# Kernel tuning notes

Hardware: AMD Instinct MI355X
Metric: run time of the kernel (lower is better)

Reference implementation:

```python
import jax, jax.numpy as jnp
import numpy as np

N = 50000
E = 800000
IN_C = 128
HID_C = 128
OUT_C = 128
N_CLS = 40


def setup_inputs() -> dict:
    key = jax.random.key(0)
    ks = jax.random.split(key, 12)
    x = jax.random.normal(ks[0], (N, IN_C), dtype=jnp.float32)
    edge_index = jax.random.randint(ks[1], (2, E), 0, N, dtype=jnp.int64)
    s = 1.0 / np.sqrt(IN_C)
    W_l1 = jax.random.uniform(ks[2], (IN_C, HID_C), jnp.float32, -s, s)
    W_r1 = jax.random.uniform(ks[3], (IN_C, HID_C), jnp.float32, -s, s)
    b1 = jax.random.uniform(ks[4], (HID_C,), jnp.float32, -s, s)
    s2 = 1.0 / np.sqrt(HID_C)
    W_l2 = jax.random.uniform(ks[5], (HID_C, OUT_C), jnp.float32, -s2, s2)
    W_r2 = jax.random.uniform(ks[6], (HID_C, OUT_C), jnp.float32, -s2, s2)
    b2 = jax.random.uniform(ks[7], (OUT_C,), jnp.float32, -s2, s2)
    s3 = 1.0 / np.sqrt(OUT_C)
    W_c = jax.random.uniform(ks[8], (OUT_C, N_CLS), jnp.float32, -s3, s3)
    b_c = jax.random.uniform(ks[9], (N_CLS,), jnp.float32, -s3, s3)
    return {"x": x, "edge_index": edge_index, "W_l1": W_l1, "W_r1": W_r1,
            "b1": b1, "W_l2": W_l2, "W_r2": W_r2, "b2": b2,
            "W_c": W_c, "b_c": b_c}


def _mean_aggregate(x, src, dst, deg_inv):
    # gather source node features over edges, scatter-mean to dst nodes
    msg = x[src]  # [E, C]
    agg = jax.ops.segment_sum(msg, dst, num_segments=N)  # [N, C]
    return agg * deg_inv[:, None]


def _sage_conv(x, src, dst, deg_inv, W_l, W_r, b):
    # PyG SAGEConv (mean aggr): out = agg @ W_l + x @ W_r + b
    agg = _mean_aggregate(x, src, dst, deg_inv)
    return agg @ W_l + x @ W_r + b


def reference(x, edge_index, W_l1, W_r1, b1, W_l2, W_r2, b2, W_c, b_c):
    src, dst = edge_index[0], edge_index[1]
    deg = jax.ops.segment_sum(jnp.ones((E,), jnp.float32), dst, num_segments=N)
    deg_inv = jnp.where(deg > 0, 1.0 / jnp.maximum(deg, 1.0), 0.0)
    h = jax.nn.relu(_sage_conv(x, src, dst, deg_inv, W_l1, W_r1, b1))
    h = jax.nn.relu(_sage_conv(h, src, dst, deg_inv, W_l2, W_r2, b2))
    return h @ W_c + b_c
```

## Files before the change

kernel.cpp:

```cpp
#include <hip/hip_runtime.h>

#define N_NODES 50000
#define N_EDGES 800000
#define C 128
#define NCLS 40
#define KB 98
#define BCAP 9216

typedef short bf16x8 __attribute__((ext_vector_type(8)));
typedef float f32x4 __attribute__((ext_vector_type(4)));
typedef unsigned short ushort_t;

__device__ __forceinline__ unsigned short f32_to_bf16(float f) {
    union { float f; unsigned u; } c; c.f = f;
    unsigned r = (c.u + 0x7FFFu + ((c.u >> 16) & 1u)) >> 16;
    return (unsigned short)r;
}
__device__ __forceinline__ float bf_lo(unsigned u) {
    union { unsigned u; float f; } c; c.u = u << 16; return c.f;
}
__device__ __forceinline__ float bf_hi(unsigned u) {
    union { unsigned u; float f; } c; c.u = u & 0xffff0000u; return c.f;
}
__device__ __forceinline__ unsigned pack_bf16(float lo, float hi) {
    return (unsigned)f32_to_bf16(lo) | ((unsigned)f32_to_bf16(hi) << 16);
}

__global__ void convert_x_kernel(const float* __restrict__ x, ushort_t* __restrict__ xb) {
    int idx = blockIdx.x * 256 + threadIdx.x;
    const float4 v0 = *(const float4*)&x[idx * 8];
    const float4 v1 = *(const float4*)&x[idx * 8 + 4];
    uint4 o;
    o.x = pack_bf16(v0.x, v0.y);
    o.y = pack_bf16(v0.z, v0.w);
    o.z = pack_bf16(v1.x, v1.y);
    o.w = pack_bf16(v1.z, v1.w);
    ((uint4*)xb)[idx] = o;
}

__global__ __launch_bounds__(256)
void bin_kernel(const int* __restrict__ src, const int* __restrict__ dst,
                int* __restrict__ bucket_cnt, unsigned* __restrict__ bucket_data) {
    __shared__ int lh[KB];
    int tid = threadIdx.x;
    int e0 = blockIdx.x * 4096;
    if (tid < KB) lh[tid] = 0;
    __syncthreads();
#pragma unroll
    for (int j = 0; j < 16; ++j) {
        int e = e0 + j * 256 + tid;
        if (e < N_EDGES) atomicAdd(&lh[dst[e] >> 9], 1);
    }
    __syncthreads();
    if (tid < KB) lh[tid] = atomicAdd(&bucket_cnt[tid], lh[tid]);
    __syncthreads();
#pragma unroll
    for (int j = 0; j < 16; ++j) {
        int e = e0 + j * 256 + tid;
        if (e < N_EDGES) {
            int d = dst[e];
            int b = d >> 9;
            int pos = atomicAdd(&lh[b], 1);
            if (pos < BCAP)
                bucket_data[b * BCAP + pos] = (unsigned)src[e] | ((unsigned)(d & 511) << 16);
        }
    }
}

__global__ __launch_bounds__(256)
void build_kernel(const int* __restrict__ bucket_cnt, const unsigned* __restrict__ bucket_data,
                  int* __restrict__ row_ptr, ushort_t* __restrict__ csr16) {
    __shared__ int wt[4];
    __shared__ int wt2[4];
    __shared__ int sbases[128];
    __shared__ int hist[512];
    __shared__ int loff[512];
    __shared__ ushort_t lcsr[BCAP];
    int tid = threadIdx.x;
    int b = blockIdx.x;
    int n0 = b << 9;
    int nb = min(512, N_NODES - n0);

    int v = 0, x = 0;
    if (tid < 128) {
        v = (tid < KB) ? bucket_cnt[tid] : 0;
        x = v;
#pragma unroll
        for (int off = 1; off < 64; off <<= 1) {
            int t = __shfl_up(x, off, 64);
            if ((tid & 63) >= off) x += t;
        }
        if ((tid & 63) == 63) wt[tid >> 6] = x;
    }
    hist[tid] = 0; hist[tid + 256] = 0;
    __syncthreads();
    if (tid < 128) sbases[tid] = x - v + ((tid >= 64) ? wt[0] : 0);
    __syncthreads();
    int base = sbases[b];
    int ecnt = min(bucket_cnt[b], BCAP);

    for (int i = tid; i < ecnt; i += 256)
        atomicAdd(&hist[bucket_data[b * BCAP + i] >> 16], 1);
    __syncthreads();

    int h0 = hist[2 * tid], h1 = hist[2 * tid + 1];
    int s = h0 + h1;
    int y = s;
#pragma unroll
    for (int off = 1; off < 64; off <<= 1) {
        int t = __shfl_up(y, off, 64);
        if ((tid & 63) >= off) y += t;
    }
    if ((tid & 63) == 63) wt2[tid >> 6] = y;
    __syncthreads();
    int add = 0;
    for (int j = 0; j < (tid >> 6); ++j) add += wt2[j];
    int ex = y + add - s;
    loff[2 * tid] = ex;
    loff[2 * tid + 1] = ex + h0;
    __syncthreads();

    for (int n = tid; n < nb; n += 256) row_ptr[n0 + n] = base + loff[n];
    if (b == KB - 1 && tid == 0) row_ptr[N_NODES] = N_EDGES;
    __syncthreads();

    for (int i = tid; i < ecnt; i += 256) {
        unsigned e = bucket_data[b * BCAP + i];
        int pos = atomicAdd(&loff[e >> 16], 1);
        lcsr[pos] = (ushort_t)(e & 0xFFFFu);
    }
    __syncthreads();
    for (int i = tid; i < ecnt; i += 256) csr16[base + i] = lcsr[i];
}

__global__ __launch_bounds__(256)
void aggregate_bf16(const ushort_t* __restrict__ feat,
                    const int* __restrict__ row_ptr,
                    const ushort_t* __restrict__ csr16,
                    ushort_t* __restrict__ agg) {
    int tid = threadIdx.x;
    int node = blockIdx.x * 16 + (tid >> 4);
    int q = tid & 15;
    if (node >= N_NODES) return;
    const uint4* fb = (const uint4*)feat;
    int beg = row_ptr[node];
    int end = row_ptr[node + 1];
    float a0[8], a1[8], a2[8], a3[8];
#pragma unroll
    for (int j = 0; j < 8; ++j) { a0[j] = 0.f; a1[j] = 0.f; a2[j] = 0.f; a3[j] = 0.f; }
    int i = beg;
    for (; i + 4 <= end; i += 4) {
        int s0 = csr16[i + 0];
        int s1 = csr16[i + 1];
        int s2 = csr16[i + 2];
        int s3 = csr16[i + 3];
        uint4 v0 = fb[s0 * 16 + q];
        uint4 v1 = fb[s1 * 16 + q];
        uint4 v2 = fb[s2 * 16 + q];
        uint4 v3 = fb[s3 * 16 + q];
        a0[0] += bf_lo(v0.x); a0[1] += bf_hi(v0.x); a0[2] += bf_lo(v0.y); a0[3] += bf_hi(v0.y);
        a0[4] += bf_lo(v0.z); a0[5] += bf_hi(v0.z); a0[6] += bf_lo(v0.w); a0[7] += bf_hi(v0.w);
        a1[0] += bf_lo(v1.x); a1[1] += bf_hi(v1.x); a1[2] += bf_lo(v1.y); a1[3] += bf_hi(v1.y);
        a1[4] += bf_lo(v1.z); a1[5] += bf_hi(v1.z); a1[6] += bf_lo(v1.w); a1[7] += bf_hi(v1.w);
        a2[0] += bf_lo(v2.x); a2[1] += bf_hi(v2.x); a2[2] += bf_lo(v2.y); a2[3] += bf_hi(v2.y);
        a2[4] += bf_lo(v2.z); a2[5] += bf_hi(v2.z); a2[6] += bf_lo(v2.w); a2[7] += bf_hi(v2.w);
        a3[0] += bf_lo(v3.x); a3[1] += bf_hi(v3.x); a3[2] += bf_lo(v3.y); a3[3] += bf_hi(v3.y);
        a3[4] += bf_lo(v3.z); a3[5] += bf_hi(v3.z); a3[6] += bf_lo(v3.w); a3[7] += bf_hi(v3.w);
    }
    int rem = end - i;
    if (rem > 0) {
        int s0 = csr16[i];
        int s1 = csr16[i + (rem > 1 ? 1 : 0)];
        int s2 = csr16[i + (rem > 2 ? 2 : 0)];
        uint4 v0 = fb[s0 * 16 + q];
        uint4 v1 = fb[s1 * 16 + q];
        uint4 v2 = fb[s2 * 16 + q];
        float m1 = rem > 1 ? 1.f : 0.f;
        float m2 = rem > 2 ? 1.f : 0.f;
        a0[0] += bf_lo(v0.x); a0[1] += bf_hi(v0.x); a0[2] += bf_lo(v0.y); a0[3] += bf_hi(v0.y);
        a0[4] += bf_lo(v0.z); a0[5] += bf_hi(v0.z); a0[6] += bf_lo(v0.w); a0[7] += bf_hi(v0.w);
        a1[0] += m1 * bf_lo(v1.x); a1[1] += m1 * bf_hi(v1.x); a1[2] += m1 * bf_lo(v1.y); a1[3] += m1 * bf_hi(v1.y);
        a1[4] += m1 * bf_lo(v1.z); a1[5] += m1 * bf_hi(v1.z); a1[6] += m1 * bf_lo(v1.w); a1[7] += m1 * bf_hi(v1.w);
        a2[0] += m2 * bf_lo(v2.x); a2[1] += m2 * bf_hi(v2.x); a2[2] += m2 * bf_lo(v2.y); a2[3] += m2 * bf_hi(v2.y);
        a2[4] += m2 * bf_lo(v2.z); a2[5] += m2 * bf_hi(v2.z); a2[6] += m2 * bf_lo(v2.w); a2[7] += m2 * bf_hi(v2.w);
    }
    int d = end - beg;
    float di = d > 0 ? 1.f / (float)d : 0.f;
    float r[8];
#pragma unroll
    for (int j = 0; j < 8; ++j) r[j] = (a0[j] + a1[j] + a2[j] + a3[j]) * di;
    uint4 o;
    o.x = pack_bf16(r[0], r[1]);
    o.y = pack_bf16(r[2], r[3]);
    o.z = pack_bf16(r[4], r[5]);
    o.w = pack_bf16(r[6], r[7]);
    ((uint4*)agg)[node * 16 + q] = o;
}

__global__ void convert_w_kernel(const float* __restrict__ Wl, const float* __restrict__ Wr,
                                 ushort_t* __restrict__ Bpre) {
    int idx = blockIdx.x * 256 + threadIdx.x;
    int n = idx >> 8;
    int k = idx & 255;
    float v = (k < 128) ? Wl[k * 128 + n] : Wr[(k - 128) * 128 + n];
    Bpre[n * 256 + k] = f32_to_bf16(v);
}

__global__ void convert_wc_kernel(const float* __restrict__ Wc, ushort_t* __restrict__ Wcb) {
    int idx = blockIdx.x * 256 + threadIdx.x;
    int n = idx >> 7;
    int k = idx & 127;
    float v = (n < NCLS) ? Wc[k * NCLS + n] : 0.f;
    Wcb[idx] = f32_to_bf16(v);
}

__global__ __launch_bounds__(256)
void sage_gemm_mfma(const ushort_t* __restrict__ agg, const ushort_t* __restrict__ xin,
                    const ushort_t* __restrict__ Bpre,
                    const float* __restrict__ bias, ushort_t* __restrict__ out) {
    __shared__ ushort_t As[64 * 40];
    __shared__ ushort_t Bs[128 * 40];
    const int tid = threadIdx.x;
    const int r0 = blockIdx.x * 64;
    const int w = tid >> 6;
    const int lane = tid & 63;
    const int m = lane & 15;
    const int quad = lane >> 4;

    f32x4 acc[8];
#pragma unroll
    for (int t = 0; t < 8; ++t) acc[t] = (f32x4){0.f, 0.f, 0.f, 0.f};

    for (int kc = 0; kc < 8; ++kc) {
        const ushort_t* Asrc = (kc < 4) ? agg : xin;
        const int kb = (kc & 3) * 32;
        {
            int row = tid >> 2;
            int kq = tid & 3;
            int rg = r0 + row; if (rg >= N_NODES) rg = N_NODES - 1;
            uint4 v = *(const uint4*)&Asrc[rg * C + kb + kq * 8];
            *(uint4*)&As[row * 40 + kq * 8] = v;
        }
#pragma unroll
        for (int i = 0; i < 2; ++i) {
            int slot = tid + i * 256;
            int n = slot >> 2;
            int qq = slot & 3;
            *(uint4*)&Bs[n * 40 + qq * 8] = *(const uint4*)&Bpre[n * 256 + kc * 32 + qq * 8];
        }
        __syncthreads();
        bf16x8 af = *(const bf16x8*)&As[(w * 16 + m) * 40 + quad * 8];
#pragma unroll
        for (int t = 0; t < 8; ++t) {
            bf16x8 bf = *(const bf16x8*)&Bs[(t * 16 + m) * 40 + quad * 8];
            acc[t] = __builtin_amdgcn_mfma_f32_16x16x32_bf16(af, bf, acc[t], 0, 0, 0);
        }
        __syncthreads();
    }
#pragma unroll
    for (int t = 0; t < 8; ++t) {
        int colv = t * 16 + m;
        float bv = bias[colv];
#pragma unroll
        for (int reg = 0; reg < 4; ++reg) {
            int rg = r0 + w * 16 + quad * 4 + reg;
            if (rg < N_NODES) {
                float vv = fmaxf(acc[t][reg] + bv, 0.f);
                out[rg * C + colv] = f32_to_bf16(vv);
            }
        }
    }
}

__global__ __launch_bounds__(256)
void classifier_mfma(const ushort_t* __restrict__ h, const ushort_t* __restrict__ Wcb,
                     const float* __restrict__ bc, float* __restrict__ out) {
    __shared__ ushort_t As4[4][64 * 40];
    __shared__ ushort_t Bs4[4][48 * 40];
    int tid = threadIdx.x;
    int r0 = blockIdx.x * 64;
    int w = tid >> 6, lane = tid & 63, m = lane & 15, quad = lane >> 4;
#pragma unroll
    for (int i = 0; i < 4; ++i) {
        int slot = tid + i * 256;
        int row = slot >> 4, kq = slot & 15;
        int rg = r0 + row; if (rg >= N_NODES) rg = N_NODES - 1;
        uint4 vv = *(const uint4*)&h[rg * C + kq * 8];
        *(uint4*)&As4[kq >> 2][row * 40 + (kq & 3) * 8] = vv;
    }
#pragma unroll
    for (int i = 0; i < 3; ++i) {
        int slot = tid + i * 256;
        int n = slot >> 4, kq = slot & 15;
        uint4 vv = *(const uint4*)&Wcb[n * C + kq * 8];
        *(uint4*)&Bs4[kq >> 2][n * 40 + (kq & 3) * 8] = vv;
    }
    __syncthreads();
    f32x4 acc[3];
#pragma unroll
    for (int t = 0; t < 3; ++t) acc[t] = (f32x4){0.f, 0.f, 0.f, 0.f};
#pragma unroll
    for (int kc = 0; kc < 4; ++kc) {
        bf16x8 af = *(const bf16x8*)&As4[kc][(w * 16 + m) * 40 + quad * 8];
#pragma unroll
        for (int t = 0; t < 3; ++t) {
            bf16x8 bf = *(const bf16x8*)&Bs4[kc][(t * 16 + m) * 40 + quad * 8];
            acc[t] = __builtin_amdgcn_mfma_f32_16x16x32_bf16(af, bf, acc[t], 0, 0, 0);
        }
    }
#pragma unroll
    for (int t = 0; t < 3; ++t) {
        int col = t * 16 + m;
        if (col < NCLS) {
            float bvv = bc[col];
#pragma unroll
            for (int reg = 0; reg < 4; ++reg) {
                int rg = r0 + w * 16 + quad * 4 + reg;
                if (rg < N_NODES) out[rg * NCLS + col] = acc[t][reg] + bvv;
            }
        }
    }
}

extern "C" void kernel_launch(void* const* d_in, const int* in_sizes, int n_in,
                              void* d_out, int out_size, void* d_ws, size_t ws_size,
                              hipStream_t stream) {
    const float* x   = (const float*)d_in[0];
    const int*   ei  = (const int*)d_in[1];
    const float* Wl1 = (const float*)d_in[2];
    const float* Wr1 = (const float*)d_in[3];
    const float* b1  = (const float*)d_in[4];
    const float* Wl2 = (const float*)d_in[5];
    const float* Wr2 = (const float*)d_in[6];
    const float* b2  = (const float*)d_in[7];
    const float* Wc  = (const float*)d_in[8];
    const float* bc  = (const float*)d_in[9];
    const int* srcI = ei;
    const int* dstI = ei + N_EDGES;
    float* out = (float*)d_out;

    ushort_t* xb   = (ushort_t*)d_ws;
    ushort_t* aggb = xb + (size_t)N_NODES * C;
    ushort_t* h1b  = aggb + (size_t)N_NODES * C;
    ushort_t* Wbf1 = h1b + (size_t)N_NODES * C;
    ushort_t* Wbf2 = Wbf1 + 32768;
    ushort_t* Wcb  = Wbf2 + 32768;
    ushort_t* csr16 = Wcb + 6144;
    int* bucket_cnt = (int*)(csr16 + N_EDGES);
    int* row_ptr    = bucket_cnt + 128;
    unsigned* bucket_data = (unsigned*)(row_ptr + N_NODES + 1);
    ushort_t* h2b = xb;

    convert_w_kernel<<<128, 256, 0, stream>>>(Wl1, Wr1, Wbf1);
    convert_w_kernel<<<128, 256, 0, stream>>>(Wl2, Wr2, Wbf2);
    convert_wc_kernel<<<24, 256, 0, stream>>>(Wc, Wcb);
    convert_x_kernel<<<(N_NODES * C / 8) / 256, 256, 0, stream>>>(x, xb);

    hipMemsetAsync(bucket_cnt, 0, 128 * sizeof(int), stream);
    bin_kernel<<<(N_EDGES + 4095) / 4096, 256, 0, stream>>>(srcI, dstI, bucket_cnt, bucket_data);
    build_kernel<<<KB, 256, 0, stream>>>(bucket_cnt, bucket_data, row_ptr, csr16);

    aggregate_bf16<<<(N_NODES + 15) / 16, 256, 0, stream>>>(xb, row_ptr, csr16, aggb);
    sage_gemm_mfma<<<(N_NODES + 63) / 64, 256, 0, stream>>>(aggb, xb, Wbf1, b1, h1b);

    aggregate_bf16<<<(N_NODES + 15) / 16, 256, 0, stream>>>(h1b, row_ptr, csr16, aggb);
    sage_gemm_mfma<<<(N_NODES + 63) / 64, 256, 0, stream>>>(aggb, h1b, Wbf2, b2, h2b);

    classifier_mfma<<<(N_NODES + 63) / 64, 256, 0, stream>>>(h2b, Wcb, bc, out);
}
```

Baseline: 228.3 us.

## Fuse aggregation, SAGE GEMM, and classifier into per-layer kernels

Merges the weight and feature conversion kernels into a single launch. Each layer now does its neighbor mean aggregation straight into shared memory and feeds that tile to the MFMA GEMM, so the aggregated tensor is never written to or read back from global memory. The second layer also runs the classifier GEMM on its shared-memory hidden tile instead of writing h2 and launching a separate kernel. In exchange each block handles 64 nodes in its gather phase (versus 16 before), which uses more shared memory per block and reduces the gather parallelism and occupancy available to hide latency.

```diff
diff --git a/kernel.cpp b/kernel.cpp
--- a/kernel.cpp
+++ b/kernel.cpp
@@ -26,16 +26,42 @@
     return (unsigned)f32_to_bf16(lo) | ((unsigned)f32_to_bf16(hi) << 16);
 }
 
-__global__ void convert_x_kernel(const float* __restrict__ x, ushort_t* __restrict__ xb) {
-    int idx = blockIdx.x * 256 + threadIdx.x;
-    const float4 v0 = *(const float4*)&x[idx * 8];
-    const float4 v1 = *(const float4*)&x[idx * 8 + 4];
-    uint4 o;
-    o.x = pack_bf16(v0.x, v0.y);
-    o.y = pack_bf16(v0.z, v0.w);
-    o.z = pack_bf16(v1.x, v1.y);
-    o.w = pack_bf16(v1.z, v1.w);
-    ((uint4*)xb)[idx] = o;
+__global__ __launch_bounds__(256)
+void convert_all(const float* __restrict__ Wl1, const float* __restrict__ Wr1,
+                 const float* __restrict__ Wl2, const float* __restrict__ Wr2,
+                 const float* __restrict__ Wc,  const float* __restrict__ x,
+                 ushort_t* __restrict__ Wbf1, ushort_t* __restrict__ Wbf2,
+                 ushort_t* __restrict__ Wcb,  ushort_t* __restrict__ xb) {
+    int b = blockIdx.x;
+    int tid = threadIdx.x;
+    if (b < 256) {
+        const float* Wl = (b < 128) ? Wl1 : Wl2;
+        const float* Wr = (b < 128) ? Wr1 : Wr2;
+        ushort_t* Bpre  = (b < 128) ? Wbf1 : Wbf2;
+        int idx = (b & 127) * 256 + tid;
+        int n = idx >> 8;
+        int k = idx & 255;
+        float v = (k < 128) ? Wl[k * 128 + n] : Wr[(k - 128) * 128 + n];
+        Bpre[n * 256 + k] = f32_to_bf16(v);
+    } else if (b < 280) {
+        int idx = (b - 256) * 256 + tid;
+        if (idx < 48 * 128) {
+            int n = idx >> 7;
+            int k = idx & 127;
+            float v = (n < NCLS) ? Wc[k * NCLS + n] : 0.f;
+            Wcb[idx] = f32_to_bf16(v);
+        }
+    } else {
+        int idx = (b - 280) * 256 + tid;
+        const float4 v0 = *(const float4*)&x[idx * 8];
+        const float4 v1 = *(const float4*)&x[idx * 8 + 4];
+        uint4 o;
+        o.x = pack_bf16(v0.x, v0.y);
+        o.y = pack_bf16(v0.z, v0.w);
+        o.z = pack_bf16(v1.x, v1.y);
+        o.w = pack_bf16(v1.z, v1.w);
+        ((uint4*)xb)[idx] = o;
+    }
 }
 
 __global__ __launch_bounds__(256)
@@ -133,190 +159,174 @@
     for (int i = tid; i < ecnt; i += 256) csr16[base + i] = lcsr[i];
 }
 
+#define ALD 136
+template<int CLS>
 __global__ __launch_bounds__(256)
-void aggregate_bf16(const ushort_t* __restrict__ feat,
-                    const int* __restrict__ row_ptr,
-                    const ushort_t* __restrict__ csr16,
-                    ushort_t* __restrict__ agg) {
-    int tid = threadIdx.x;
-    int node = blockIdx.x * 16 + (tid >> 4);
-    int q = tid & 15;
-    if (node >= N_NODES) return;
-    const uint4* fb = (const uint4*)feat;
-    int beg = row_ptr[node];
-    int end = row_ptr[node + 1];
-    float a0[8], a1[8], a2[8], a3[8];
-#pragma unroll
-    for (int j = 0; j < 8; ++j) { a0[j] = 0.f; a1[j] = 0.f; a2[j] = 0.f; a3[j] = 0.f; }
-    int i = beg;
-    for (; i + 4 <= end; i += 4) {
-        int s0 = csr16[i + 0];
-        int s1 = csr16[i + 1];
-        int s2 = csr16[i + 2];
-        int s3 = csr16[i + 3];
-        uint4 v0 = fb[s0 * 16 + q];
-        uint4 v1 = fb[s1 * 16 + q];
-        uint4 v2 = fb[s2 * 16 + q];
-        uint4 v3 = fb[s3 * 16 + q];
-        a0[0] += bf_lo(v0.x); a0[1] += bf_hi(v0.x); a0[2] += bf_lo(v0.y); a0[3] += bf_hi(v0.y);
-        a0[4] += bf_lo(v0.z); a0[5] += bf_hi(v0.z); a0[6] += bf_lo(v0.w); a0[7] += bf_hi(v0.w);
-        a1[0] += bf_lo(v1.x); a1[1] += bf_hi(v1.x); a1[2] += bf_lo(v1.y); a1[3] += bf_hi(v1.y);
-        a1[4] += bf_lo(v1.z); a1[5] += bf_hi(v1.z); a1[6] += bf_lo(v1.w); a1[7] += bf_hi(v1.w);
-        a2[0] += bf_lo(v2.x); a2[1] += bf_hi(v2.x); a2[2] += bf_lo(v2.y); a2[3] += bf_hi(v2.y);
-        a2[4] += bf_lo(v2.z); a2[5] += bf_hi(v2.z); a2[6] += bf_lo(v2.w); a2[7] += bf_hi(v2.w);
-        a3[0] += bf_lo(v3.x); a3[1] += bf_hi(v3.x); a3[2] += bf_lo(v3.y); a3[3] += bf_hi(v3.y);
-        a3[4] += bf_lo(v3.z); a3[5] += bf_hi(v3.z); a3[6] += bf_lo(v3.w); a3[7] += bf_hi(v3.w);
-    }
-    int rem = end - i;
-    if (rem > 0) {
-        int s0 = csr16[i];
-        int s1 = csr16[i + (rem > 1 ? 1 : 0)];
-        int s2 = csr16[i + (rem > 2 ? 2 : 0)];
-        uint4 v0 = fb[s0 * 16 + q];
-        uint4 v1 = fb[s1 * 16 + q];
-        uint4 v2 = fb[s2 * 16 + q];
-        float m1 = rem > 1 ? 1.f : 0.f;
-        float m2 = rem > 2 ? 1.f : 0.f;
-        a0[0] += bf_lo(v0.x); a0[1] += bf_hi(v0.x); a0[2] += bf_lo(v0.y); a0[3] += bf_hi(v0.y);
-        a0[4] += bf_lo(v0.z); a0[5] += bf_hi(v0.z); a0[6] += bf_lo(v0.w); a0[7] += bf_hi(v0.w);
-        a1[0] += m1 * bf_lo(v1.x); a1[1] += m1 * bf_hi(v1.x); a1[2] += m1 * bf_lo(v1.y); a1[3] += m1 * bf_hi(v1.y);
-        a1[4] += m1 * bf_lo(v1.z); a1[5] += m1 * bf_hi(v1.z); a1[6] += m1 * bf_lo(v1.w); a1[7] += m1 * bf_hi(v1.w);
-        a2[0] += m2 * bf_lo(v2.x); a2[1] += m2 * bf_hi(v2.x); a2[2] += m2 * bf_lo(v2.y); a2[3] += m2 * bf_hi(v2.y);
-        a2[4] += m2 * bf_lo(v2.z); a2[5] += m2 * bf_hi(v2.z); a2[6] += m2 * bf_lo(v2.w); a2[7] += m2 * bf_hi(v2.w);
-    }
-    int d = end - beg;
-    float di = d > 0 ? 1.f / (float)d : 0.f;
-    float r[8];
-#pragma unroll
-    for (int j = 0; j < 8; ++j) r[j] = (a0[j] + a1[j] + a2[j] + a3[j]) * di;
-    uint4 o;
-    o.x = pack_bf16(r[0], r[1]);
-    o.y = pack_bf16(r[2], r[3]);
-    o.z = pack_bf16(r[4], r[5]);
-    o.w = pack_bf16(r[6], r[7]);
-    ((uint4*)agg)[node * 16 + q] = o;
-}
-
-__global__ void convert_w_kernel(const float* __restrict__ Wl, const float* __restrict__ Wr,
-                                 ushort_t* __restrict__ Bpre) {
-    int idx = blockIdx.x * 256 + threadIdx.x;
-    int n = idx >> 8;
-    int k = idx & 255;
-    float v = (k < 128) ? Wl[k * 128 + n] : Wr[(k - 128) * 128 + n];
-    Bpre[n * 256 + k] = f32_to_bf16(v);
-}
-
-__global__ void convert_wc_kernel(const float* __restrict__ Wc, ushort_t* __restrict__ Wcb) {
-    int idx = blockIdx.x * 256 + threadIdx.x;
-    int n = idx >> 7;
-    int k = idx & 127;
-    float v = (n < NCLS) ? Wc[k * NCLS + n] : 0.f;
-    Wcb[idx] = f32_to_bf16(v);
-}
-
-__global__ __launch_bounds__(256)
-void sage_gemm_mfma(const ushort_t* __restrict__ agg, const ushort_t* __restrict__ xin,
-                    const ushort_t* __restrict__ Bpre,
-                    const float* __restrict__ bias, ushort_t* __restrict__ out) {
-    __shared__ ushort_t As[64 * 40];
-    __shared__ ushort_t Bs[128 * 40];
+void fused_layer(const ushort_t* __restrict__ feat,
+                 const int* __restrict__ row_ptr,
+                 const ushort_t* __restrict__ csr16,
+                 const ushort_t* __restrict__ Bpre,
+                 const float* __restrict__ bias,
+                 ushort_t* __restrict__ hout,
+                 const ushort_t* __restrict__ Wcb,
+                 const float* __restrict__ bc,
+                 float* __restrict__ out) {
+    __shared__ ushort_t aggL[64 * ALD];
+    __shared__ ushort_t stg[64 * 40 + 128 * 40];
+    ushort_t* AsX = stg;
+    ushort_t* BsP = stg + 64 * 40;
     const int tid = threadIdx.x;
     const int r0 = blockIdx.x * 64;
-    const int w = tid >> 6;
-    const int lane = tid & 63;
-    const int m = lane & 15;
-    const int quad = lane >> 4;
+    const int w = tid >> 6, lane = tid & 63, m = lane & 15, quad = lane >> 4;
+
+    const uint4* fb = (const uint4*)feat;
+    const int q = tid & 15;
+    for (int p = 0; p < 4; ++p) {
+        int nl = p * 16 + (tid >> 4);
+        int node = r0 + nl;
+        int beg = 0, end = 0;
+        if (node < N_NODES) { beg = row_ptr[node]; end = row_ptr[node + 1]; }
+        float a0[8], a1[8], a2[8], a3[8];
+#pragma unroll
+        for (int j = 0; j < 8; ++j) { a0[j] = 0.f; a1[j] = 0.f; a2[j] = 0.f; a3[j] = 0.f; }
+        int i = beg;
+        for (; i + 4 <= end; i += 4) {
+            int s0 = csr16[i + 0];
+            int s1 = csr16[i + 1];
+            int s2 = csr16[i + 2];
+            int s3 = csr16[i + 3];
+            uint4 v0 = fb[s0 * 16 + q];
+            uint4 v1 = fb[s1 * 16 + q];
+            uint4 v2 = fb[s2 * 16 + q];
+            uint4 v3 = fb[s3 * 16 + q];
+            a0[0] += bf_lo(v0.x); a0[1] += bf_hi(v0.x); a0[2] += bf_lo(v0.y); a0[3] += bf_hi(v0.y);
+            a0[4] += bf_lo(v0.z); a0[5] += bf_hi(v0.z); a0[6] += bf_lo(v0.w); a0[7] += bf_hi(v0.w);
+            a1[0] += bf_lo(v1.x); a1[1] += bf_hi(v1.x); a1[2] += bf_lo(v1.y); a1[3] += bf_hi(v1.y);
+            a1[4] += bf_lo(v1.z); a1[5] += bf_hi(v1.z); a1[6] += bf_lo(v1.w); a1[7] += bf_hi(v1.w);
+            a2[0] += bf_lo(v2.x); a2[1] += bf_hi(v2.x); a2[2] += bf_lo(v2.y); a2[3] += bf_hi(v2.y);
+            a2[4] += bf_lo(v2.z); a2[5] += bf_hi(v2.z); a2[6] += bf_lo(v2.w); a2[7] += bf_hi(v2.w);
+            a3[0] += bf_lo(v3.x); a3[1] += bf_hi(v3.x); a3[2] += bf_lo(v3.y); a3[3] += bf_hi(v3.y);
+            a3[4] += bf_lo(v3.z); a3[5] += bf_hi(v3.z); a3[6] += bf_lo(v3.w); a3[7] += bf_hi(v3.w);
+        }
+        int rem = end - i;
+        if (rem > 0) {
+            int s0 = csr16[i];
+            int s1 = csr16[i + (rem > 1 ? 1 : 0)];
+            int s2 = csr16[i + (rem > 2 ? 2 : 0)];
+            uint4 v0 = fb[s0 * 16 + q];
+            uint4 v1 = fb[s1 * 16 + q];
+            uint4 v2 = fb[s2 * 16 + q];
+            float m1 = rem > 1 ? 1.f : 0.f;
+            float m2 = rem > 2 ? 1.f : 0.f;
+            a0[0] += bf_lo(v0.x); a0[1] += bf_hi(v0.x); a0[2] += bf_lo(v0.y); a0[3] += bf_hi(v0.y);
+            a0[4] += bf_lo(v0.z); a0[5] += bf_hi(v0.z); a0[6] += bf_lo(v0.w); a0[7] += bf_hi(v0.w);
+            a1[0] += m1 * bf_lo(v1.x); a1[1] += m1 * bf_hi(v1.x); a1[2] += m1 * bf_lo(v1.y); a1[3] += m1 * bf_hi(v1.y);
+            a1[4] += m1 * bf_lo(v1.z); a1[5] += m1 * bf_hi(v1.z); a1[6] += m1 * bf_lo(v1.w); a1[7] += m1 * bf_hi(v1.w);
+            a2[0] += m2 * bf_lo(v2.x); a2[1] += m2 * bf_hi(v2.x); a2[2] += m2 * bf_lo(v2.y); a2[3] += m2 * bf_hi(v2.y);
+            a2[4] += m2 * bf_lo(v2.z); a2[5] += m2 * bf_hi(v2.z); a2[6] += m2 * bf_lo(v2.w); a2[7] += m2 * bf_hi(v2.w);
+        }
+        int d = end - beg;
+        float di = d > 0 ? 1.f / (float)d : 0.f;
+        float r[8];
+#pragma unroll
+        for (int j = 0; j < 8; ++j) r[j] = (a0[j] + a1[j] + a2[j] + a3[j]) * di;
+        uint4 o;
+        o.x = pack_bf16(r[0], r[1]);
+        o.y = pack_bf16(r[2], r[3]);
+        o.z = pack_bf16(r[4], r[5]);
+        o.w = pack_bf16(r[6], r[7]);
+        *(uint4*)&aggL[nl * ALD + q * 8] = o;
+    }
+    __syncthreads();
 
     f32x4 acc[8];
 #pragma unroll
     for (int t = 0; t < 8; ++t) acc[t] = (f32x4){0.f, 0.f, 0.f, 0.f};
 
     for (int kc = 0; kc < 8; ++kc) {
-        const ushort_t* Asrc = (kc < 4) ? agg : xin;
-        const int kb = (kc & 3) * 32;
-        {
+        if (kc) __syncthreads();
+        if (kc >= 4) {
             int row = tid >> 2;
             int kq = tid & 3;
             int rg = r0 + row; if (rg >= N_NODES) rg = N_NODES - 1;
-            uint4 v = *(const uint4*)&Asrc[rg * C + kb + kq * 8];
-            *(uint4*)&As[row * 40 + kq * 8] = v;
+            uint4 v = *(const uint4*)&feat[rg * C + (kc & 3) * 32 + kq * 8];
+            *(uint4*)&AsX[row * 40 + kq * 8] = v;
         }
 #pragma unroll
         for (int i = 0; i < 2; ++i) {
             int slot = tid + i * 256;
             int n = slot >> 2;
             int qq = slot & 3;
-            *(uint4*)&Bs[n * 40 + qq * 8] = *(const uint4*)&Bpre[n * 256 + kc * 32 + qq * 8];
+            *(uint4*)&BsP[n * 40 + qq * 8] = *(const uint4*)&Bpre[n * 256 + kc * 32 + qq * 8];
         }
         __syncthreads();
-        bf16x8 af = *(const bf16x8*)&As[(w * 16 + m) * 40 + quad * 8];
+        bf16x8 af = (kc < 4)
+            ? *(const bf16x8*)&aggL[(w * 16 + m) * ALD + kc * 32 + quad * 8]
+            : *(const bf16x8*)&AsX[(w * 16 + m) * 40 + quad * 8];
 #pragma unroll
         for (int t = 0; t < 8; ++t) {
-            bf16x8 bf = *(const bf16x8*)&Bs[(t * 16 + m) * 40 + quad * 8];
+            bf16x8 bf = *(const bf16x8*)&BsP[(t * 16 + m) * 40 + quad * 8];
             acc[t] = __builtin_amdgcn_mfma_f32_16x16x32_bf16(af, bf, acc[t], 0, 0, 0);
         }
-        __syncthreads();
-    }
-#pragma unroll
-    for (int t = 0; t < 8; ++t) {
-        int colv = t * 16 + m;
-        float bv = bias[colv];
-#pragma unroll
-        for (int reg = 0; reg < 4; ++reg) {
-            int rg = r0 + w * 16 + quad * 4 + reg;
-            if (rg < N_NODES) {
-                float vv = fmaxf(acc[t][reg] + bv, 0.f);
-                out[rg * C + colv] = f32_to_bf16(vv);
-            }
-        }
-    }
-}
-
-__global__ __launch_bounds__(256)
-void classifier_mfma(const ushort_t* __restrict__ h, const ushort_t* __restrict__ Wcb,
-                     const float* __restrict__ bc, float* __restrict__ out) {
-    __shared__ ushort_t As4[4][64 * 40];
-    __shared__ ushort_t Bs4[4][48 * 40];
-    int tid = threadIdx.x;
-    int r0 = blockIdx.x * 64;
-    int w = tid >> 6, lane = tid & 63, m = lane & 15, quad = lane >> 4;
-#pragma unroll
-    for (int i = 0; i < 4; ++i) {
-        int slot = tid + i * 256;
-        int row = slot >> 4, kq = slot & 15;
-        int rg = r0 + row; if (rg >= N_NODES) rg = N_NODES - 1;
-        uint4 vv = *(const uint4*)&h[rg * C + kq * 8];
-        *(uint4*)&As4[kq >> 2][row * 40 + (kq & 3) * 8] = vv;
-    }
-#pragma unroll
-    for (int i = 0; i < 3; ++i) {
-        int slot = tid + i * 256;
-        int n = slot >> 4, kq = slot & 15;
-        uint4 vv = *(const uint4*)&Wcb[n * C + kq * 8];
-        *(uint4*)&Bs4[kq >> 2][n * 40 + (kq & 3) * 8] = vv;
-    }
-    __syncthreads();
-    f32x4 acc[3];
-#pragma unroll
-    for (int t = 0; t < 3; ++t) acc[t] = (f32x4){0.f, 0.f, 0.f, 0.f};
-#pragma unroll
-    for (int kc = 0; kc < 4; ++kc) {
-        bf16x8 af = *(const bf16x8*)&As4[kc][(w * 16 + m) * 40 + quad * 8];
-#pragma unroll
-        for (int t = 0; t < 3; ++t) {
-            bf16x8 bf = *(const bf16x8*)&Bs4[kc][(t * 16 + m) * 40 + quad * 8];
-            acc[t] = __builtin_amdgcn_mfma_f32_16x16x32_bf16(af, bf, acc[t], 0, 0, 0);
-        }
-    }
-#pragma unroll
-    for (int t = 0; t < 3; ++t) {
-        int col = t * 16 + m;
-        if (col < NCLS) {
-            float bvv = bc[col];
+    }
+
+    if (CLS == 0) {
+#pragma unroll
+        for (int t = 0; t < 8; ++t) {
+            int colv = t * 16 + m;
+            float bv = bias[colv];
 #pragma unroll
             for (int reg = 0; reg < 4; ++reg) {
                 int rg = r0 + w * 16 + quad * 4 + reg;
-                if (rg < N_NODES) out[rg * NCLS + col] = acc[t][reg] + bvv;
+                if (rg < N_NODES) {
+                    float vv = fmaxf(acc[t][reg] + bv, 0.f);
+                    hout[rg * C + colv] = f32_to_bf16(vv);
+                }
+            }
+        }
+    } else {
+        __syncthreads();
+#pragma unroll
+        for (int t = 0; t < 8; ++t) {
+            int colv = t * 16 + m;
+            float bv = bias[colv];
+#pragma unroll
+            for (int reg = 0; reg < 4; ++reg) {
+                int rl = w * 16 + quad * 4 + reg;
+                float vv = fmaxf(acc[t][reg] + bv, 0.f);
+                aggL[rl * ALD + colv] = f32_to_bf16(vv);
+            }
+        }
+#pragma unroll
+        for (int i = 0; i < 3; ++i) {
+            int slot = tid + i * 256;
+            int n = slot >> 4, kq = slot & 15;
+            uint4 vv = *(const uint4*)&Wcb[n * C + kq * 8];
+            *(uint4*)&stg[(kq >> 2) * (48 * 40) + n * 40 + (kq & 3) * 8] = vv;
+        }
+        __syncthreads();
+        f32x4 acc2[3];
+#pragma unroll
+        for (int t = 0; t < 3; ++t) acc2[t] = (f32x4){0.f, 0.f, 0.f, 0.f};
+#pragma unroll
+        for (int kc = 0; kc < 4; ++kc) {
+            bf16x8 af = *(const bf16x8*)&aggL[(w * 16 + m) * ALD + kc * 32 + quad * 8];
+#pragma unroll
+            for (int t = 0; t < 3; ++t) {
+                bf16x8 bf = *(const bf16x8*)&stg[kc * (48 * 40) + (t * 16 + m) * 40 + quad * 8];
+                acc2[t] = __builtin_amdgcn_mfma_f32_16x16x32_bf16(af, bf, acc2[t], 0, 0, 0);
+            }
+        }
+#pragma unroll
+        for (int t = 0; t < 3; ++t) {
+            int col = t * 16 + m;
+            if (col < NCLS) {
+                float bvv = bc[col];
+#pragma unroll
+                for (int reg = 0; reg < 4; ++reg) {
+                    int rg = r0 + w * 16 + quad * 4 + reg;
+                    if (rg < N_NODES) out[rg * NCLS + col] = acc2[t][reg] + bvv;
+                }
             }
         }
     }
@@ -340,8 +350,7 @@
     float* out = (float*)d_out;
 
     ushort_t* xb   = (ushort_t*)d_ws;
-    ushort_t* aggb = xb + (size_t)N_NODES * C;
-    ushort_t* h1b  = aggb + (size_t)N_NODES * C;
+    ushort_t* h1b  = xb + (size_t)N_NODES * C;
     ushort_t* Wbf1 = h1b + (size_t)N_NODES * C;
     ushort_t* Wbf2 = Wbf1 + 32768;
     ushort_t* Wcb  = Wbf2 + 32768;
@@ -349,22 +358,17 @@
     int* bucket_cnt = (int*)(csr16 + N_EDGES);
     int* row_ptr    = bucket_cnt + 128;
     unsigned* bucket_data = (unsigned*)(row_ptr + N_NODES + 1);
-    ushort_t* h2b = xb;
-
-    convert_w_kernel<<<128, 256, 0, stream>>>(Wl1, Wr1, Wbf1);
-    convert_w_kernel<<<128, 256, 0, stream>>>(Wl2, Wr2, Wbf2);
-    convert_wc_kernel<<<24, 256, 0, stream>>>(Wc, Wcb);
-    convert_x_kernel<<<(N_NODES * C / 8) / 256, 256, 0, stream>>>(x, xb);
+
+    convert_all<<<280 + (N_NODES * C / 8 + 255) / 256, 256, 0, stream>>>(
+        Wl1, Wr1, Wl2, Wr2, Wc, x, Wbf1, Wbf2, Wcb, xb);
 
     hipMemsetAsync(bucket_cnt, 0, 128 * sizeof(int), stream);
     bin_kernel<<<(N_EDGES + 4095) / 4096, 256, 0, stream>>>(srcI, dstI, bucket_cnt, bucket_data);
     build_kernel<<<KB, 256, 0, stream>>>(bucket_cnt, bucket_data, row_ptr, csr16);
 
-    aggregate_bf16<<<(N_NODES + 15) / 16, 256, 0, stream>>>(xb, row_ptr, csr16, aggb);
-    sage_gemm_mfma<<<(N_NODES + 63) / 64, 256, 0, stream>>>(aggb, xb, Wbf1, b1, h1b);
-
-    aggregate_bf16<<<(N_NODES + 15) / 16, 256, 0, stream>>>(h1b, row_ptr, csr16, aggb);
-    sage_gemm_mfma<<<(N_NODES + 63) / 64, 256, 0, stream>>>(aggb, h1b, Wbf2, b2, h2b);
-
-    classifier_mfma<<<(N_NODES + 63) / 64, 256, 0, stream>>>(h2b, Wcb, bc, out);
-}
+    fused_layer<0><<<(N_NODES + 63) / 64, 256, 0, stream>>>(
+        xb, row_ptr, csr16, Wbf1, b1, h1b, nullptr, nullptr, nullptr);
+
+    fused_layer<1><<<(N_NODES + 63) / 64, 256, 0, stream>>>(
+        h1b, row_ptr, csr16, Wbf2, b2, nullptr, Wcb, bc, out);
+}
```

Result: faster. 205.7 us (median of 2 runs) (-9.9%).
